# Performance work log

Hardware: AMD Instinct MI355X
Metric: run time of the kernel (lower is better)

The kernel has to match this reference:

```python
import jax, jax.numpy as jnp
import numpy as np

B, S, D = 8, 4096, 64
NEG = 10000.0


def setup_inputs() -> dict:
    key = jax.random.key(0)
    k1, k2, k3, k4 = jax.random.split(key, 4)
    query = jax.random.normal(k1, (B, S, D), dtype=jnp.float32)
    k_ = jax.random.normal(k2, (B, S, D), dtype=jnp.float32)
    v_ = jax.random.normal(k3, (B, S, D), dtype=jnp.float32)
    # padding mask [B, Sk]: mostly valid, tail padded for some rows
    lens = jax.random.randint(k4, (B,), S // 2, S + 1)
    mask = jnp.arange(S)[None, :] < lens[:, None]
    return {"query": query, "key": k_, "value": v_, "mask": mask}


def reference(query, key, value, mask):
    d = query.shape[-1]
    scale = 1.0 / jnp.sqrt(jnp.asarray(d, dtype=query.dtype))
    # e: [B, Sq, Sk]
    e = jnp.einsum("bqd,bkd->bqk", query, key) * scale
    # causal (history_only) mask: key index > query index gets -10000
    q_idx = jnp.arange(query.shape[1])[:, None]
    k_idx = jnp.arange(key.shape[1])[None, :]
    e = e - NEG * (k_idx > q_idx).astype(e.dtype)[None, :, :]
    # padding mask [B, 1, Sk]
    e = e - NEG * (1.0 - mask.astype(e.dtype))[:, None, :]
    attention = jax.nn.softmax(e, axis=-1)
    return jnp.einsum("bqk,bkd->bqd", attention, value)
```

## Files before the change

kernel.cpp:

```cpp
#include <hip/hip_runtime.h>
#include <hip/hip_bf16.h>

#define B_N 8
#define S_N 4096
#define D_N 64
#define BK 64
#define NQT 64
#define TILE_BYTES 8192

typedef __attribute__((ext_vector_type(8))) short bf16x8;
typedef __attribute__((ext_vector_type(4))) float f32x4;
typedef __attribute__((ext_vector_type(16))) float f32x16;
typedef unsigned uint2v __attribute__((ext_vector_type(2)));

__device__ __forceinline__ float fast_exp2(float x) {
#if __has_builtin(__builtin_amdgcn_exp2f)
  return __builtin_amdgcn_exp2f(x);
#else
  return exp2f(x);
#endif
}

__device__ __forceinline__ unsigned f2bf_u(float x) {
  __hip_bfloat16 h = __float2bfloat16(x);
  return (unsigned)__builtin_bit_cast(unsigned short, h);
}
__device__ __forceinline__ unsigned pack2(float a, float b) {
  return f2bf_u(a) | (f2bf_u(b) << 16);
}
__device__ __forceinline__ int swzoff(int row, int colb) {
  return row * 128 + (colb ^ ((((row & 7) ^ ((row >> 3) & 7))) << 4));
}

__device__ __forceinline__ void pl32swap(unsigned& a, unsigned& b) {
#if __has_builtin(__builtin_amdgcn_permlane32_swap)
  uint2v r = __builtin_amdgcn_permlane32_swap(a, b, false, false);
  a = r[0];
  b = r[1];
#else
  asm volatile("v_permlane32_swap_b32 %0, %1" : "+v"(a), "+v"(b));
#endif
}
__device__ __forceinline__ float xhalf_max(float x) {
  unsigned a = __builtin_bit_cast(unsigned, x), b = a;
  pl32swap(a, b);
  return fmaxf(__builtin_bit_cast(float, a), __builtin_bit_cast(float, b));
}
__device__ __forceinline__ float xhalf_sum(float x) {
  unsigned a = __builtin_bit_cast(unsigned, x), b = a;
  pl32swap(a, b);
  return __builtin_bit_cast(float, a) + __builtin_bit_cast(float, b);
}

#define GLOAD(g, l)                                                  \
  __builtin_amdgcn_global_load_lds(                                  \
      (const __attribute__((address_space(1))) unsigned*)(g),        \
      (__attribute__((address_space(3))) unsigned*)(l), 16, 0, 0)

__global__ void __launch_bounds__(256)
prep_kernel(const float* __restrict__ K, const float* __restrict__ V,
            const unsigned* __restrict__ mask, char* __restrict__ Ks,
            char* __restrict__ VTs, int* __restrict__ lens) {
  __shared__ float vl[64][72];
  const int bt = blockIdx.x, tid = threadIdx.x;
  const int b = bt >> 6, kt = bt & 63;

  if (tid < 64) {
    unsigned first = mask[0];
    bool v;
    int gi = kt * 64 + tid;
    if (first == 0x01010101u) {
      v = ((const unsigned char*)mask)[(size_t)b * S_N + gi] != 0;
    } else if (first == 0x3F800000u) {
      v = ((const float*)mask)[(size_t)b * S_N + gi] != 0.0f;
    } else {
      v = ((const int*)mask)[(size_t)b * S_N + gi] != 0;
    }
    unsigned long long bal = __ballot(v);
    if (tid == 0) atomicAdd(&lens[b], __popcll(bal));
  }

  const float* Kt = K + (size_t)bt * 4096;
  const float* Vt = V + (size_t)bt * 4096;
  char* Ko = Ks + (size_t)bt * TILE_BYTES;
  char* Vo = VTs + (size_t)bt * TILE_BYTES;
#pragma unroll
  for (int i = 0; i < 2; ++i) {
    int c = tid + i * 256;
    int r = c >> 3, j = c & 7;
    f32x4 a = *(const f32x4*)(Kt + r * 64 + j * 8);
    f32x4 b4 = *(const f32x4*)(Kt + r * 64 + j * 8 + 4);
    union { bf16x8 v; unsigned u[4]; } pk;
    pk.u[0] = pack2(a[0], a[1]);   pk.u[1] = pack2(a[2], a[3]);
    pk.u[2] = pack2(b4[0], b4[1]); pk.u[3] = pack2(b4[2], b4[3]);
    *(bf16x8*)(Ko + swzoff(r, j * 16)) = pk.v;
    f32x4 va = *(const f32x4*)(Vt + r * 64 + j * 8);
    f32x4 vb = *(const f32x4*)(Vt + r * 64 + j * 8 + 4);
#pragma unroll
    for (int e = 0; e < 4; ++e) vl[j * 8 + e][r] = va[e];
#pragma unroll
    for (int e = 0; e < 4; ++e) vl[j * 8 + 4 + e][r] = vb[e];
  }
  __syncthreads();
#pragma unroll
  for (int i = 0; i < 2; ++i) {
    int c = tid + i * 256;
    int d = c >> 3, j = c & 7;
    f32x4 fa = *(const f32x4*)(&vl[d][j * 8]);
    f32x4 fb = *(const f32x4*)(&vl[d][j * 8 + 4]);
    union { bf16x8 v; unsigned u[4]; } pk;
    pk.u[0] = pack2(fa[0], fa[1]); pk.u[1] = pack2(fa[2], fa[3]);
    pk.u[2] = pack2(fb[0], fb[1]); pk.u[3] = pack2(fb[2], fb[3]);
    *(bf16x8*)(Vo + swzoff(d, j * 16)) = pk.v;
  }
}

#define MERGE_OFF 32768

__global__ void __launch_bounds__(256)
attn_kernel(const float* __restrict__ Qg, const char* __restrict__ Ks,
            const char* __restrict__ VTs, const int* __restrict__ lens,
            float* __restrict__ Og) {
  __shared__ __align__(16) char sm[65536];
  const int tid = threadIdx.x;
  const int bid = blockIdx.x;
  const int b = bid & 7;
  const int qt = (NQT - 1) - (bid >> 3);
  const int q0 = qt * 64;
  const int len = lens[b];
  int nt = (len + BK - 1) >> 6;
  if (qt + 1 < nt) nt = qt + 1;

  const int lane = tid & 63;
  const int w = tid >> 6;
  const int p = w >> 1;
  const int ws = w & 1;
  const int q31 = lane & 31;
  const int h = lane >> 5;
  const int qg = q0 + ws * 32 + q31;

  char* pbase = sm + p * 32768;
  const char* Kb = Ks + (size_t)(b * NQT) * TILE_BYTES;
  const char* Vb = VTs + (size_t)(b * NQT) * TILE_BYTES;
  const char* srcb = ws ? Vb : Kb;

  auto issue = [&](int t, int bf) {
    const char* s = srcb + (size_t)t * TILE_BYTES + lane * 16;
    char* d = pbase + bf * 16384 + ws * 8192;
#pragma unroll
    for (int i = 0; i < 8; ++i) GLOAD(s + i * 1024, d + i * 1024);
  };

  const int ntp = (nt - p + 1) >> 1;
  const int jmax = (nt + 1) >> 1;

  if (ntp > 0) issue(p, 0);

  constexpr float CS = 0.125f * 1.4426950408889634f;
  bf16x8 qf[4];
#pragma unroll
  for (int c = 0; c < 4; ++c) {
    const float* src = Qg + ((size_t)(b * S_N) + qg) * D_N + c * 16 + h * 8;
    f32x4 a = *(const f32x4*)src;
    f32x4 b4 = *(const f32x4*)(src + 4);
    union { bf16x8 v; unsigned u[4]; } pk;
    pk.u[0] = pack2(a[0] * CS, a[1] * CS);
    pk.u[1] = pack2(a[2] * CS, a[3] * CS);
    pk.u[2] = pack2(b4[0] * CS, b4[1] * CS);
    pk.u[3] = pack2(b4[2] * CS, b4[3] * CS);
    qf[c] = pk.v;
  }

  f32x16 ot0 = {}, ot1 = {};
  float m = -30000.0f, l = 0.0f;

  for (int j = 0; j < jmax; ++j) {
    asm volatile("s_waitcnt vmcnt(0)" ::: "memory");
    __builtin_amdgcn_sched_barrier(0);
    __builtin_amdgcn_s_barrier();
    __builtin_amdgcn_sched_barrier(0);

    const bool active = j < ntp;
    if (active && (j + 1) < ntp) issue(2 * (j + 1) + p, (j + 1) & 1);
    if (!active) continue;

    const int t = 2 * j + p;
    const char* kbase = pbase + (j & 1) * 16384;
    const char* vbase = kbase + 8192;

    bf16x8 kf[8], vf[8];
#pragma unroll
    for (int c = 0; c < 4; ++c) {
      kf[c]     = *(const bf16x8*)(kbase + swzoff(q31, c * 32 + h * 16));
      kf[4 + c] = *(const bf16x8*)(kbase + swzoff(32 + q31, c * 32 + h * 16));
      vf[c]     = *(const bf16x8*)(vbase + swzoff(q31, c * 32 + h * 16));
      vf[4 + c] = *(const bf16x8*)(vbase + swzoff(32 + q31, c * 32 + h * 16));
    }

    f32x16 s0 = {}, s1 = {};
    __builtin_amdgcn_s_setprio(1);
#pragma unroll
    for (int c = 0; c < 4; ++c) {
      s0 = __builtin_amdgcn_mfma_f32_32x32x16_bf16(kf[c], qf[c], s0, 0, 0, 0);
      s1 = __builtin_amdgcn_mfma_f32_32x32x16_bf16(kf[4 + c], qf[c], s1, 0, 0, 0);
    }
    __builtin_amdgcn_s_setprio(0);

    const int kv0 = t * BK;
    if (t == nt - 1) {
#pragma unroll
      for (int g = 0; g < 4; ++g)
#pragma unroll
        for (int jj = 0; jj < 4; ++jj) {
          int kl = 8 * g + 4 * h + jj;
          if (kv0 + kl > qg || kv0 + kl >= len) s0[g * 4 + jj] = -30000.0f;
          if (kv0 + 32 + kl > qg || kv0 + 32 + kl >= len) s1[g * 4 + jj] = -30000.0f;
        }
    }

    float rmax = s0[0];
#pragma unroll
    for (int i = 1; i < 16; ++i) rmax = fmaxf(rmax, s0[i]);
#pragma unroll
    for (int i = 0; i < 16; ++i) rmax = fmaxf(rmax, s1[i]);
    rmax = xhalf_max(rmax);
    if (!__all(rmax <= m + 8.0f)) {
      float mn = fmaxf(m, rmax);
      float alpha = fast_exp2(m - mn);
      m = mn;
      l *= alpha;
#pragma unroll
      for (int i = 0; i < 16; ++i) { ot0[i] *= alpha; ot1[i] *= alpha; }
    }
    float ps0 = 0.f, ps1 = 0.f, ps2 = 0.f, ps3 = 0.f;
#pragma unroll
    for (int g = 0; g < 4; ++g) {
      s0[4 * g + 0] = fast_exp2(s0[4 * g + 0] - m); ps0 += s0[4 * g + 0];
      s0[4 * g + 1] = fast_exp2(s0[4 * g + 1] - m); ps1 += s0[4 * g + 1];
      s0[4 * g + 2] = fast_exp2(s0[4 * g + 2] - m); ps2 += s0[4 * g + 2];
      s0[4 * g + 3] = fast_exp2(s0[4 * g + 3] - m); ps3 += s0[4 * g + 3];
      s1[4 * g + 0] = fast_exp2(s1[4 * g + 0] - m); ps0 += s1[4 * g + 0];
      s1[4 * g + 1] = fast_exp2(s1[4 * g + 1] - m); ps1 += s1[4 * g + 1];
      s1[4 * g + 2] = fast_exp2(s1[4 * g + 2] - m); ps2 += s1[4 * g + 2];
      s1[4 * g + 3] = fast_exp2(s1[4 * g + 3] - m); ps3 += s1[4 * g + 3];
    }
    l += xhalf_sum((ps0 + ps1) + (ps2 + ps3));

    unsigned opk0[4][2], opk1[4][2];
#pragma unroll
    for (int g = 0; g < 4; ++g) {
      opk0[g][0] = pack2(s0[4 * g + 0], s0[4 * g + 1]);
      opk0[g][1] = pack2(s0[4 * g + 2], s0[4 * g + 3]);
      opk1[g][0] = pack2(s1[4 * g + 0], s1[4 * g + 1]);
      opk1[g][1] = pack2(s1[4 * g + 2], s1[4 * g + 3]);
    }
    bf16x8 pb[4];
#pragma unroll
    for (int c = 0; c < 4; ++c) {
      const unsigned(*o)[2] = (c < 2) ? opk0 : opk1;
      const int g0 = 2 * (c & 1), g1 = g0 + 1;
      unsigned a0 = o[g0][0], b0 = o[g1][0];
      unsigned a1 = o[g0][1], b1 = o[g1][1];
      pl32swap(a0, b0);
      pl32swap(a1, b1);
      union { bf16x8 v; unsigned u[4]; } pk;
      pk.u[0] = a0; pk.u[1] = a1; pk.u[2] = b0; pk.u[3] = b1;
      pb[c] = pk.v;
    }

    __builtin_amdgcn_s_setprio(1);
#pragma unroll
    for (int c = 0; c < 4; ++c) {
      ot0 = __builtin_amdgcn_mfma_f32_32x32x16_bf16(vf[c], pb[c], ot0, 0, 0, 0);
      ot1 = __builtin_amdgcn_mfma_f32_32x32x16_bf16(vf[4 + c], pb[c], ot1, 0, 0, 0);
    }
    __builtin_amdgcn_s_setprio(0);
  }

  __builtin_amdgcn_sched_barrier(0);
  __builtin_amdgcn_s_barrier();
  __builtin_amdgcn_sched_barrier(0);
  if (p == 1) {
    float* rec = (float*)(sm + MERGE_OFF + (size_t)(ws * 64 + lane) * 144);
#pragma unroll
    for (int g = 0; g < 4; ++g) {
      *(f32x4*)(rec + 4 * g) =
          (f32x4){ot0[4 * g], ot0[4 * g + 1], ot0[4 * g + 2], ot0[4 * g + 3]};
      *(f32x4*)(rec + 16 + 4 * g) =
          (f32x4){ot1[4 * g], ot1[4 * g + 1], ot1[4 * g + 2], ot1[4 * g + 3]};
    }
    rec[32] = m;
    rec[33] = l;
  }
  __builtin_amdgcn_sched_barrier(0);
  __builtin_amdgcn_s_barrier();
  __builtin_amdgcn_sched_barrier(0);
  if (p == 0) {
    const float* rec = (const float*)(sm + MERGE_OFF + (size_t)(ws * 64 + lane) * 144);
    float m1 = rec[32], l1 = rec[33];
    float mx = fmaxf(m, m1);
    float a0 = fast_exp2(m - mx), a1 = fast_exp2(m1 - mx);
    float linv = 1.0f / (l * a0 + l1 * a1);
    float* orow = Og + ((size_t)(b * S_N) + qg) * D_N;
#pragma unroll
    for (int g = 0; g < 4; ++g) {
      f32x4 r0 = *(const f32x4*)(rec + 4 * g);
      f32x4 r1 = *(const f32x4*)(rec + 16 + 4 * g);
      f32x4 oa = {(ot0[4 * g] * a0 + r0[0] * a1) * linv,
                  (ot0[4 * g + 1] * a0 + r0[1] * a1) * linv,
                  (ot0[4 * g + 2] * a0 + r0[2] * a1) * linv,
                  (ot0[4 * g + 3] * a0 + r0[3] * a1) * linv};
      *(f32x4*)(orow + 8 * g + 4 * h) = oa;
      f32x4 ob = {(ot1[4 * g] * a0 + r1[0] * a1) * linv,
                  (ot1[4 * g + 1] * a0 + r1[1] * a1) * linv,
                  (ot1[4 * g + 2] * a0 + r1[2] * a1) * linv,
                  (ot1[4 * g + 3] * a0 + r1[3] * a1) * linv};
      *(f32x4*)(orow + 32 + 8 * g + 4 * h) = ob;
    }
  }
}

extern "C" void kernel_launch(void* const* d_in, const int* in_sizes, int n_in,
                              void* d_out, int out_size, void* d_ws, size_t ws_size,
                              hipStream_t stream) {
  const float* Qg = (const float*)d_in[0];
  const float* Kg = (const float*)d_in[1];
  const float* Vg = (const float*)d_in[2];
  const unsigned* mask = (const unsigned*)d_in[3];
  float* Og = (float*)d_out;

  int* lens = (int*)d_ws;
  char* Ks = (char*)d_ws + 4096;
  char* VTs = Ks + (size_t)B_N * NQT * TILE_BYTES;

  hipMemsetAsync(lens, 0, B_N * sizeof(int), stream);
  prep_kernel<<<dim3(B_N * NQT), dim3(256), 0, stream>>>(Kg, Vg, mask, Ks, VTs, lens);
  attn_kernel<<<dim3(B_N * NQT), dim3(256), 0, stream>>>(Qg, Ks, VTs, lens, Og);
}
```

Baseline: 65.23 us.

## Split KV loop across four wave-pairs per block with single-buffered register prefetch

Doubles the block to 512 threads so four wave-pairs each take every fourth KV tile, where before two pairs each took every other tile. Each pair now has one LDS buffer: it copies the tile into registers, hits a barrier, then issues the next tile's load. At the end the four partial softmax states are merged through LDS. This shortens the per-block serial KV loop for long causal rows and reorders the q-tile-to-block mapping, at the cost of a larger block, an extra barrier per step and a bigger merge.

```diff
diff --git a/kernel.cpp b/kernel.cpp
--- a/kernel.cpp
+++ b/kernel.cpp
@@ -115,17 +115,18 @@
   }
 }
 
-#define MERGE_OFF 32768
-
-__global__ void __launch_bounds__(256)
+__global__ void __launch_bounds__(512, 4)
 attn_kernel(const float* __restrict__ Qg, const char* __restrict__ Ks,
             const char* __restrict__ VTs, const int* __restrict__ lens,
             float* __restrict__ Og) {
   __shared__ __align__(16) char sm[65536];
   const int tid = threadIdx.x;
   const int bid = blockIdx.x;
-  const int b = bid & 7;
-  const int qt = (NQT - 1) - (bid >> 3);
+  const int half = bid >> 8;
+  const int idx = bid & 255;
+  const int b = idx & 7;
+  const int rr = idx >> 3;
+  const int qt = half ? rr : 63 - rr;
   const int q0 = qt * 64;
   const int len = lens[b];
   int nt = (len + BK - 1) >> 6;
@@ -139,22 +140,22 @@
   const int h = lane >> 5;
   const int qg = q0 + ws * 32 + q31;
 
-  char* pbase = sm + p * 32768;
+  char* pbase = sm + p * 16384;
   const char* Kb = Ks + (size_t)(b * NQT) * TILE_BYTES;
   const char* Vb = VTs + (size_t)(b * NQT) * TILE_BYTES;
   const char* srcb = ws ? Vb : Kb;
 
-  auto issue = [&](int t, int bf) {
+  auto issue = [&](int t) {
     const char* s = srcb + (size_t)t * TILE_BYTES + lane * 16;
-    char* d = pbase + bf * 16384 + ws * 8192;
+    char* d = pbase + ws * 8192;
 #pragma unroll
     for (int i = 0; i < 8; ++i) GLOAD(s + i * 1024, d + i * 1024);
   };
 
-  const int ntp = (nt - p + 1) >> 1;
-  const int jmax = (nt + 1) >> 1;
-
-  if (ntp > 0) issue(p, 0);
+  const int ntp = (nt > p) ? ((nt - p + 3) >> 2) : 0;
+  const int jmax = (nt + 3) >> 2;
+
+  if (ntp > 0) issue(p);
 
   constexpr float CS = 0.125f * 1.4426950408889634f;
   bf16x8 qf[4];
@@ -181,21 +182,27 @@
     __builtin_amdgcn_sched_barrier(0);
 
     const bool active = j < ntp;
-    if (active && (j + 1) < ntp) issue(2 * (j + 1) + p, (j + 1) & 1);
+    bf16x8 kf[8], vf[8];
+    if (active) {
+      const char* kbase = pbase;
+      const char* vbase = pbase + 8192;
+#pragma unroll
+      for (int c = 0; c < 4; ++c) {
+        kf[c]     = *(const bf16x8*)(kbase + swzoff(q31, c * 32 + h * 16));
+        kf[4 + c] = *(const bf16x8*)(kbase + swzoff(32 + q31, c * 32 + h * 16));
+        vf[c]     = *(const bf16x8*)(vbase + swzoff(q31, c * 32 + h * 16));
+        vf[4 + c] = *(const bf16x8*)(vbase + swzoff(32 + q31, c * 32 + h * 16));
+      }
+      asm volatile("s_waitcnt lgkmcnt(0)" ::: "memory");
+      __builtin_amdgcn_sched_barrier(0);
+    }
+    __builtin_amdgcn_s_barrier();
+    __builtin_amdgcn_sched_barrier(0);
     if (!active) continue;
 
-    const int t = 2 * j + p;
-    const char* kbase = pbase + (j & 1) * 16384;
-    const char* vbase = kbase + 8192;
-
-    bf16x8 kf[8], vf[8];
-#pragma unroll
-    for (int c = 0; c < 4; ++c) {
-      kf[c]     = *(const bf16x8*)(kbase + swzoff(q31, c * 32 + h * 16));
-      kf[4 + c] = *(const bf16x8*)(kbase + swzoff(32 + q31, c * 32 + h * 16));
-      vf[c]     = *(const bf16x8*)(vbase + swzoff(q31, c * 32 + h * 16));
-      vf[4 + c] = *(const bf16x8*)(vbase + swzoff(32 + q31, c * 32 + h * 16));
-    }
+    if (j + 1 < ntp) issue(4 * (j + 1) + p);
+
+    const int t = 4 * j + p;
 
     f32x16 s0 = {}, s1 = {};
     __builtin_amdgcn_s_setprio(1);
@@ -280,8 +287,9 @@
   __builtin_amdgcn_sched_barrier(0);
   __builtin_amdgcn_s_barrier();
   __builtin_amdgcn_sched_barrier(0);
-  if (p == 1) {
-    float* rec = (float*)(sm + MERGE_OFF + (size_t)(ws * 64 + lane) * 144);
+  const int ridx = (ws * 32 + q31) * 2 + h;
+  if (p != 0) {
+    float* rec = (float*)sm + ((p - 1) * 128 + ridx) * 36;
 #pragma unroll
     for (int g = 0; g < 4; ++g) {
       *(f32x4*)(rec + 4 * g) =
@@ -296,25 +304,27 @@
   __builtin_amdgcn_s_barrier();
   __builtin_amdgcn_sched_barrier(0);
   if (p == 0) {
-    const float* rec = (const float*)(sm + MERGE_OFF + (size_t)(ws * 64 + lane) * 144);
-    float m1 = rec[32], l1 = rec[33];
-    float mx = fmaxf(m, m1);
+    const float* r0 = (const float*)sm + (0 * 128 + ridx) * 36;
+    const float* r1 = (const float*)sm + (1 * 128 + ridx) * 36;
+    const float* r2 = (const float*)sm + (2 * 128 + ridx) * 36;
+    float m1 = r0[32], m2 = r1[32], m3 = r2[32];
+    float mx = fmaxf(fmaxf(m, m1), fmaxf(m2, m3));
     float a0 = fast_exp2(m - mx), a1 = fast_exp2(m1 - mx);
-    float linv = 1.0f / (l * a0 + l1 * a1);
+    float a2 = fast_exp2(m2 - mx), a3 = fast_exp2(m3 - mx);
+    float linv = 1.0f / (l * a0 + r0[33] * a1 + r1[33] * a2 + r2[33] * a3);
     float* orow = Og + ((size_t)(b * S_N) + qg) * D_N;
 #pragma unroll
     for (int g = 0; g < 4; ++g) {
-      f32x4 r0 = *(const f32x4*)(rec + 4 * g);
-      f32x4 r1 = *(const f32x4*)(rec + 16 + 4 * g);
-      f32x4 oa = {(ot0[4 * g] * a0 + r0[0] * a1) * linv,
-                  (ot0[4 * g + 1] * a0 + r0[1] * a1) * linv,
-                  (ot0[4 * g + 2] * a0 + r0[2] * a1) * linv,
-                  (ot0[4 * g + 3] * a0 + r0[3] * a1) * linv};
+      f32x4 p1a = *(const f32x4*)(r0 + 4 * g), p1b = *(const f32x4*)(r0 + 16 + 4 * g);
+      f32x4 p2a = *(const f32x4*)(r1 + 4 * g), p2b = *(const f32x4*)(r1 + 16 + 4 * g);
+      f32x4 p3a = *(const f32x4*)(r2 + 4 * g), p3b = *(const f32x4*)(r2 + 16 + 4 * g);
+      f32x4 oa, ob;
+#pragma unroll
+      for (int e = 0; e < 4; ++e) {
+        oa[e] = (ot0[4 * g + e] * a0 + p1a[e] * a1 + p2a[e] * a2 + p3a[e] * a3) * linv;
+        ob[e] = (ot1[4 * g + e] * a0 + p1b[e] * a1 + p2b[e] * a2 + p3b[e] * a3) * linv;
+      }
       *(f32x4*)(orow + 8 * g + 4 * h) = oa;
-      f32x4 ob = {(ot1[4 * g] * a0 + r1[0] * a1) * linv,
-                  (ot1[4 * g + 1] * a0 + r1[1] * a1) * linv,
-                  (ot1[4 * g + 2] * a0 + r1[2] * a1) * linv,
-                  (ot1[4 * g + 3] * a0 + r1[3] * a1) * linv};
       *(f32x4*)(orow + 32 + 8 * g + 4 * h) = ob;
     }
   }
@@ -335,5 +345,5 @@
 
   hipMemsetAsync(lens, 0, B_N * sizeof(int), stream);
   prep_kernel<<<dim3(B_N * NQT), dim3(256), 0, stream>>>(Kg, Vg, mask, Ks, VTs, lens);
-  attn_kernel<<<dim3(B_N * NQT), dim3(256), 0, stream>>>(Qg, Ks, VTs, lens, Og);
-}
+  attn_kernel<<<dim3(B_N * NQT), dim3(512), 0, stream>>>(Qg, Ks, VTs, lens, Og);
+}
```

Result: slower. 132.3 us (+102.8%).

## Single-buffer K/V tiles in LDS to halve shared memory and remap query tiles

Applied to the files above, without the earlier changes.

Shared memory is halved by dropping the double buffer. Each iteration now reads K/V fragments into registers, waits on LDS, and barriers before issuing the next tile's global-to-LDS load into the same buffer. This is meant to let more blocks fit per CU. The merge scratch now reuses the low LDS region, and the block index is remapped so a second half of the grid processes query tiles in ascending order. In exchange, the next tile's load can no longer overlap the current tile's register loads, and there is an extra barrier per iteration.

```diff
diff --git a/kernel.cpp b/kernel.cpp
--- a/kernel.cpp
+++ b/kernel.cpp
@@ -115,17 +115,18 @@
   }
 }
 
-#define MERGE_OFF 32768
-
 __global__ void __launch_bounds__(256)
 attn_kernel(const float* __restrict__ Qg, const char* __restrict__ Ks,
             const char* __restrict__ VTs, const int* __restrict__ lens,
             float* __restrict__ Og) {
-  __shared__ __align__(16) char sm[65536];
+  __shared__ __align__(16) char sm[32768];
   const int tid = threadIdx.x;
   const int bid = blockIdx.x;
-  const int b = bid & 7;
-  const int qt = (NQT - 1) - (bid >> 3);
+  const int half = bid >> 8;
+  const int idx = bid & 255;
+  const int b = idx & 7;
+  const int rr = idx >> 3;
+  const int qt = half ? rr : 63 - rr;
   const int q0 = qt * 64;
   const int len = lens[b];
   int nt = (len + BK - 1) >> 6;
@@ -139,22 +140,22 @@
   const int h = lane >> 5;
   const int qg = q0 + ws * 32 + q31;
 
-  char* pbase = sm + p * 32768;
+  char* pbase = sm + p * 16384;
   const char* Kb = Ks + (size_t)(b * NQT) * TILE_BYTES;
   const char* Vb = VTs + (size_t)(b * NQT) * TILE_BYTES;
   const char* srcb = ws ? Vb : Kb;
 
-  auto issue = [&](int t, int bf) {
+  auto issue = [&](int t) {
     const char* s = srcb + (size_t)t * TILE_BYTES + lane * 16;
-    char* d = pbase + bf * 16384 + ws * 8192;
+    char* d = pbase + ws * 8192;
 #pragma unroll
     for (int i = 0; i < 8; ++i) GLOAD(s + i * 1024, d + i * 1024);
   };
 
-  const int ntp = (nt - p + 1) >> 1;
+  const int ntp = (nt > p) ? ((nt - p + 1) >> 1) : 0;
   const int jmax = (nt + 1) >> 1;
 
-  if (ntp > 0) issue(p, 0);
+  if (ntp > 0) issue(p);
 
   constexpr float CS = 0.125f * 1.4426950408889634f;
   bf16x8 qf[4];
@@ -181,21 +182,27 @@
     __builtin_amdgcn_sched_barrier(0);
 
     const bool active = j < ntp;
-    if (active && (j + 1) < ntp) issue(2 * (j + 1) + p, (j + 1) & 1);
+    bf16x8 kf[8], vf[8];
+    if (active) {
+      const char* kbase = pbase;
+      const char* vbase = pbase + 8192;
+#pragma unroll
+      for (int c = 0; c < 4; ++c) {
+        kf[c]     = *(const bf16x8*)(kbase + swzoff(q31, c * 32 + h * 16));
+        kf[4 + c] = *(const bf16x8*)(kbase + swzoff(32 + q31, c * 32 + h * 16));
+        vf[c]     = *(const bf16x8*)(vbase + swzoff(q31, c * 32 + h * 16));
+        vf[4 + c] = *(const bf16x8*)(vbase + swzoff(32 + q31, c * 32 + h * 16));
+      }
+      asm volatile("s_waitcnt lgkmcnt(0)" ::: "memory");
+      __builtin_amdgcn_sched_barrier(0);
+    }
+    __builtin_amdgcn_s_barrier();
+    __builtin_amdgcn_sched_barrier(0);
     if (!active) continue;
 
+    if (j + 1 < ntp) issue(2 * (j + 1) + p);
+
     const int t = 2 * j + p;
-    const char* kbase = pbase + (j & 1) * 16384;
-    const char* vbase = kbase + 8192;
-
-    bf16x8 kf[8], vf[8];
-#pragma unroll
-    for (int c = 0; c < 4; ++c) {
-      kf[c]     = *(const bf16x8*)(kbase + swzoff(q31, c * 32 + h * 16));
-      kf[4 + c] = *(const bf16x8*)(kbase + swzoff(32 + q31, c * 32 + h * 16));
-      vf[c]     = *(const bf16x8*)(vbase + swzoff(q31, c * 32 + h * 16));
-      vf[4 + c] = *(const bf16x8*)(vbase + swzoff(32 + q31, c * 32 + h * 16));
-    }
 
     f32x16 s0 = {}, s1 = {};
     __builtin_amdgcn_s_setprio(1);
@@ -280,8 +287,9 @@
   __builtin_amdgcn_sched_barrier(0);
   __builtin_amdgcn_s_barrier();
   __builtin_amdgcn_sched_barrier(0);
+  const int ridx = (ws * 32 + q31) * 2 + h;
   if (p == 1) {
-    float* rec = (float*)(sm + MERGE_OFF + (size_t)(ws * 64 + lane) * 144);
+    float* rec = (float*)(sm + (size_t)ridx * 144);
 #pragma unroll
     for (int g = 0; g < 4; ++g) {
       *(f32x4*)(rec + 4 * g) =
@@ -296,7 +304,7 @@
   __builtin_amdgcn_s_barrier();
   __builtin_amdgcn_sched_barrier(0);
   if (p == 0) {
-    const float* rec = (const float*)(sm + MERGE_OFF + (size_t)(ws * 64 + lane) * 144);
+    const float* rec = (const float*)(sm + (size_t)ridx * 144);
     float m1 = rec[32], l1 = rec[33];
     float mx = fmaxf(m, m1);
     float a0 = fast_exp2(m - mx), a1 = fast_exp2(m1 - mx);
```

After: 63.22 us. 1.03x faster.
